# Kernel tuning notes

Hardware: AMD Instinct MI355X
Metric: run time of the kernel (lower is better)

Reference implementation:

```python
import jax, jax.numpy as jnp
import numpy as np

NODE_DIM = 256
HID = 128
EDGE_DIM = 128
NUM_BINS = 22
MAX_LEN = 2056
TOTAL_FEATS = HID * 3 + NUM_BINS * 2 + 2


def get_index_embedding(indices, embed_size, max_len):
    # sinusoidal index embedding as in RiboFlow utils
    K = jnp.arange(embed_size // 2, dtype=jnp.float32)
    ang = indices[..., None].astype(jnp.float32) * jnp.pi / (max_len ** (2.0 * K / embed_size))
    return jnp.concatenate([jnp.sin(ang), jnp.cos(ang)], axis=-1)


def calc_distogram(pos, min_bin, max_bin, num_bins):
    # pos: [B, N, 3] -> one-hot distogram [B, N, N, num_bins]
    d = jnp.linalg.norm(pos[:, :, None, :] - pos[:, None, :, :], axis=-1)[..., None]
    lower = jnp.linspace(min_bin, max_bin, num_bins)
    upper = jnp.concatenate([lower[1:], jnp.array([1e8], dtype=jnp.float32)])
    return ((d > lower) & (d < upper)).astype(jnp.float32)


def cross_concat(f):
    # f: [B, N, D] -> [B, N, N, 2D] via row/col tiling
    B, N, D = f.shape
    return jnp.concatenate([
        jnp.broadcast_to(f[:, :, None, :], (B, N, N, D)),
        jnp.broadcast_to(f[:, None, :, :], (B, N, N, D)),
    ], axis=-1)


def _linear_params(key, fi, fo):
    s = 1.0 / np.sqrt(fi)
    kw, kb = jax.random.split(key)
    W = jax.random.uniform(kw, (fi, fo), jnp.float32, -s, s)
    b = jax.random.uniform(kb, (fo,), jnp.float32, -s, s)
    return W, b


def setup_inputs() -> dict:
    key = jax.random.key(0)
    ks = jax.random.split(key, 12)
    B, N = 1, 512
    inp = {
        'node_features': jax.random.normal(ks[0], (B, N, NODE_DIM), jnp.float32),
        'trans': jax.random.normal(ks[1], (B, N, 3), jnp.float32) * 10.0,
        'sc_trans': jax.random.normal(ks[2], (B, N, 3), jnp.float32) * 10.0,
        'edge_mask': jnp.ones((B, N, N), jnp.float32),
        'flow_mask': (jax.random.uniform(ks[4], (B, N)) > 0.5).astype(jnp.float32),
    }
    inp['W_n2e'], inp['b_n2e'] = _linear_params(ks[5], NODE_DIM, HID)
    inp['W_rp'], inp['b_rp'] = _linear_params(ks[6], HID, HID)
    inp['W1'], inp['b1'] = _linear_params(ks[7], TOTAL_FEATS, EDGE_DIM)
    inp['W2'], inp['b2'] = _linear_params(ks[8], EDGE_DIM, EDGE_DIM)
    inp['W3'], inp['b3'] = _linear_params(ks[9], EDGE_DIM, EDGE_DIM)
    inp['ln_g'] = jnp.ones((EDGE_DIM,), jnp.float32)
    inp['ln_b'] = jnp.zeros((EDGE_DIM,), jnp.float32)
    return inp


def reference(node_features, trans, sc_trans, edge_mask, flow_mask,
              W_n2e, b_n2e, W_rp, b_rp, W1, b1, W2, b2, W3, b3, ln_g, ln_b):
    B, N, _ = node_features.shape
    # node -> edge projection, then cross-concat tiling: [B,N,N,2*HID]
    n2e = node_features @ W_n2e + b_n2e
    pair_node_feats = cross_concat(n2e)
    # relative position sinusoidal embedding + linear: [B,N,N,HID]
    seq = jnp.arange(N, dtype=jnp.float32)
    relpos = jnp.broadcast_to(seq[None, :, None] - seq[None, None, :], (B, N, N))
    relpos_feats = get_index_embedding(relpos, HID, MAX_LEN) @ W_rp + b_rp
    # distograms: [B,N,N,NUM_BINS] each
    dist_feats = calc_distogram(trans, 0.001, 20.0, NUM_BINS)
    sc_feats = calc_distogram(sc_trans, 0.001, 20.0, NUM_BINS)
    # flow mask pair features: [B,N,N,2]
    flow_feat = cross_concat(flow_mask[..., None])
    feats = jnp.concatenate([pair_node_feats, relpos_feats, dist_feats, sc_feats, flow_feat], axis=-1)
    # 3-layer MLP + LayerNorm
    h = jax.nn.relu(feats @ W1 + b1)
    h = jax.nn.relu(h @ W2 + b2)
    h = h @ W3 + b3
    mu = jnp.mean(h, axis=-1, keepdims=True)
    var = jnp.var(h, axis=-1, keepdims=True)
    h = (h - mu) * jax.lax.rsqrt(var + 1e-5) * ln_g + ln_b
    return h * edge_mask[..., None]
```

## Files before the change

kernel.cpp:

```cpp
#include <hip/hip_runtime.h>


using bf16x8 = __attribute__((ext_vector_type(8))) short;
using f32x4  = __attribute__((ext_vector_type(4))) float;

__device__ __forceinline__ unsigned short f2bf(float f) {
    unsigned int u;
    __builtin_memcpy(&u, &f, 4);
    unsigned int r = (u + 0x7fffu + ((u >> 16) & 1u)) >> 16;
    return (unsigned short)r;
}

__device__ __forceinline__ unsigned int cvt_pk_bf16(float lo, float hi) {
    unsigned int r;
    asm("v_cvt_pk_bf16_f32 %0, %1, %2" : "=v"(r) : "v"(lo), "v"(hi));
    return r;
}

__global__ void pre_all(const float* __restrict__ nf,
                        const float* __restrict__ Wn2e,
                        const float* __restrict__ bn2e,
                        const float* __restrict__ W1,
                        const float* __restrict__ b1,
                        const float* __restrict__ flow,
                        const float* __restrict__ Wrp,
                        const float* __restrict__ brp,
                        const float* __restrict__ W2,
                        const float* __restrict__ W3,
                        float* __restrict__ A, float* __restrict__ Bv,
                        float* __restrict__ Rm,
                        short* __restrict__ W2b, short* __restrict__ W3b)
{
    __shared__ float s0[256];
    __shared__ float s1[128];
    const int bid = blockIdx.x;
    const int m = threadIdx.x;

    if (bid < 512) {
        const int i = bid;
        s0[m]       = nf[i * 256 + m];
        s0[m + 128] = nf[i * 256 + 128 + m];
        __syncthreads();
        float c0 = 0.f, c1 = 0.f, c2 = 0.f, c3 = 0.f;
        #pragma unroll 4
        for (int k = 0; k < 256; k += 4) {
            c0 += s0[k + 0] * Wn2e[(k + 0) * 128 + m];
            c1 += s0[k + 1] * Wn2e[(k + 1) * 128 + m];
            c2 += s0[k + 2] * Wn2e[(k + 2) * 128 + m];
            c3 += s0[k + 3] * Wn2e[(k + 3) * 128 + m];
        }
        s1[m] = bn2e[m] + ((c0 + c1) + (c2 + c3));
        __syncthreads();
        const float fl = flow[i];
        float aA0 = b1[m] + fl * W1[428 * 128 + m], aA1 = 0.f;
        float aB0 =         fl * W1[429 * 128 + m], aB1 = 0.f;
        #pragma unroll 4
        for (int k = 0; k < 128; k += 2) {
            aA0 += s1[k]     * W1[(k) * 128 + m];
            aA1 += s1[k + 1] * W1[(k + 1) * 128 + m];
            aB0 += s1[k]     * W1[(128 + k) * 128 + m];
            aB1 += s1[k + 1] * W1[(129 + k) * 128 + m];
        }
        A[i * 128 + m]  = aA0 + aA1;
        Bv[i * 128 + m] = aB0 + aB1;
    } else if (bid < 1535) {
        const int dix = bid - 512;
        const float d = (float)(dix - 511);
        const int K = m & 63;
        const float denom = powf(2056.0f, (float)K * (1.0f / 64.0f));
        const float ang = d * 3.14159265358979323846f / denom;
        s0[m] = (m < 64) ? sinf(ang) : cosf(ang);
        __syncthreads();
        float c0 = 0.f, c1 = 0.f, c2 = 0.f, c3 = 0.f;
        #pragma unroll 4
        for (int k = 0; k < 128; k += 4) {
            c0 += s0[k + 0] * Wrp[(k + 0) * 128 + m];
            c1 += s0[k + 1] * Wrp[(k + 1) * 128 + m];
            c2 += s0[k + 2] * Wrp[(k + 2) * 128 + m];
            c3 += s0[k + 3] * Wrp[(k + 3) * 128 + m];
        }
        s1[m] = brp[m] + ((c0 + c1) + (c2 + c3));
        __syncthreads();
        c0 = 0.f; c1 = 0.f; c2 = 0.f; c3 = 0.f;
        #pragma unroll 4
        for (int k = 0; k < 128; k += 4) {
            c0 += s1[k + 0] * W1[(256 + k) * 128 + m];
            c1 += s1[k + 1] * W1[(257 + k) * 128 + m];
            c2 += s1[k + 2] * W1[(258 + k) * 128 + m];
            c3 += s1[k + 3] * W1[(259 + k) * 128 + m];
        }
        Rm[dix * 128 + m] = (c0 + c1) + (c2 + c3);
    } else {
        const int t = (bid - 1535) * 128 + m;
        for (int h = 0; h < 2; h++) {
            const int idx = t + h * 8192;
            const int k = idx >> 7, n = idx & 127;
            const int dst = ((k >> 3) * 128 + n) * 8 + (k & 7);
            W2b[dst] = (short)f2bf(W2[idx]);
            W3b[dst] = (short)f2bf(W3[idx]);
        }
    }
}

__global__ __launch_bounds__(512, 4) void edge_main(
    const float* __restrict__ trans,
    const float* __restrict__ sctrans,
    const float* __restrict__ emask,
    const float* __restrict__ W1,
    const short* __restrict__ W2b,
    const float* __restrict__ b2,
    const short* __restrict__ W3b,
    const float* __restrict__ b3,
    const float* __restrict__ lng,
    const float* __restrict__ lnb,
    const float* __restrict__ A,
    const float* __restrict__ Bv,
    const float* __restrict__ Rm,
    float* __restrict__ out)
{
    __shared__ __align__(16) short W2L[16384];
    __shared__ __align__(16) short W3L[16384];
    __shared__ __align__(16) float As[128];
    __shared__ int binsD[256];
    __shared__ int binsS[256];

    const int tid = threadIdx.x;
    const int i  = blockIdx.x >> 1;
    const int j0 = (blockIdx.x & 1) << 8;

    for (int r = 0; r < 4; r++) {
        const int off = (r * 512 + tid) * 16;
        __builtin_amdgcn_global_load_lds(
            (const __attribute__((address_space(1))) void*)((const char*)W2b + off),
            (__attribute__((address_space(3))) void*)((char*)W2L + off), 16, 0, 0);
        __builtin_amdgcn_global_load_lds(
            (const __attribute__((address_space(1))) void*)((const char*)W3b + off),
            (__attribute__((address_space(3))) void*)((char*)W3L + off), 16, 0, 0);
    }

    if (tid < 128) As[tid] = A[i * 128 + tid];

    {
        const int p = tid & 255;
        const float* P = (tid < 256) ? trans : sctrans;
        const int j = j0 + p;
        const float dx = __fsub_rn(P[i * 3 + 0], P[j * 3 + 0]);
        const float dy = __fsub_rn(P[i * 3 + 1], P[j * 3 + 1]);
        const float dz = __fsub_rn(P[i * 3 + 2], P[j * 3 + 2]);
        const float d2 = __fadd_rn(__fadd_rn(__fmul_rn(dx, dx), __fmul_rn(dy, dy)),
                                   __fmul_rn(dz, dz));
        const double dd = (double)sqrtf(d2);
        const double step = (20.0 - 0.001) / 21.0;
        int bin = -1;
        for (int b = 0; b < 22; b++) {
            const double lo = (b == 21) ? 20.0 : __dadd_rn(0.001, __dmul_rn((double)b, step));
            const double up = (b == 20) ? 20.0 :
                              ((b == 21) ? 1e8 : __dadd_rn(0.001, __dmul_rn((double)(b + 1), step)));
            if (dd > lo && dd < up) bin = b;
        }
        if (tid < 256) binsD[p] = bin; else binsS[p] = bin;
    }
    __syncthreads();

    const int w = tid >> 6;
    const int l = tid & 63;
    const int q = l >> 4;
    const int ln16 = l & 15;

    const f32x4 vzero = {0.0f, 0.0f, 0.0f, 0.0f};
    const int laA = (((q & 1) * 2) * 16 + ln16) * 4;
    const int laB = laA + 64;
    const bool selHi = (q >> 1) != 0;

    for (int mt = 0; mt < 2; mt++) {
        const int p = 32 * w + mt * 16 + ln16;
        const int j = j0 + p;

        bf16x8 af[4];
        {
            const int didx = i - j + 511;
            const int bD = binsD[p], bS = binsS[p];
            const float sD = bD >= 0 ? 1.0f : 0.0f;
            const float sS = bS >= 0 ? 1.0f : 0.0f;
            const int rD = 384 + (bD >= 0 ? bD : 0);
            const int rS = 406 + (bS >= 0 ? bS : 0);
            const float* __restrict__ BvR = &Bv[j * 128];
            const float* __restrict__ RmR = &Rm[didx * 128];
            const float* __restrict__ WdR = &W1[rD * 128];
            const float* __restrict__ WsR = &W1[rS * 128];
            #pragma unroll
            for (int kb = 0; kb < 4; kb++) {
                const int f0 = kb * 32 + q * 8;
                const f32x4 bv0 = *(const f32x4*)&BvR[f0];
                const f32x4 bv1 = *(const f32x4*)&BvR[f0 + 4];
                const f32x4 r0  = *(const f32x4*)&RmR[f0];
                const f32x4 r1  = *(const f32x4*)&RmR[f0 + 4];
                const f32x4 a0  = *(const f32x4*)&As[f0];
                const f32x4 a1  = *(const f32x4*)&As[f0 + 4];
                const f32x4 w0  = *(const f32x4*)&WdR[f0];
                const f32x4 w1  = *(const f32x4*)&WdR[f0 + 4];
                const f32x4 s0  = *(const f32x4*)&WsR[f0];
                const f32x4 s1  = *(const f32x4*)&WsR[f0 + 4];
                float h[8];
                #pragma unroll
                for (int e = 0; e < 4; e++) {
                    h[e]     = fmaxf(a0[e] + bv0[e] + r0[e] + sD * w0[e] + sS * s0[e], 0.0f);
                    h[e + 4] = fmaxf(a1[e] + bv1[e] + r1[e] + sD * w1[e] + sS * s1[e], 0.0f);
                }
                union { unsigned int u[4]; bf16x8 v; } cv;
                cv.u[0] = cvt_pk_bf16(h[0], h[1]);
                cv.u[1] = cvt_pk_bf16(h[2], h[3]);
                cv.u[2] = cvt_pk_bf16(h[4], h[5]);
                cv.u[3] = cvt_pk_bf16(h[6], h[7]);
                af[kb] = cv.v;
            }
        }

        unsigned int P[8][2];
        #pragma unroll
        for (int nt = 0; nt < 8; nt++) {
            f32x4 acc2 = vzero;
            #pragma unroll
            for (int kb = 0; kb < 4; kb++) {
                const bf16x8 wf = *(const bf16x8*)&W2L[((kb * 4 + q) * 128 + nt * 16 + ln16) * 8];
                acc2 = __builtin_amdgcn_mfma_f32_16x16x32_bf16(wf, af[kb], acc2, 0, 0, 0);
            }
            const f32x4 b2c = *(const f32x4*)&b2[nt * 16 + q * 4];
            P[nt][0] = cvt_pk_bf16(fmaxf(acc2[0] + b2c[0], 0.0f),
                                   fmaxf(acc2[1] + b2c[1], 0.0f));
            P[nt][1] = cvt_pk_bf16(fmaxf(acc2[2] + b2c[2], 0.0f),
                                   fmaxf(acc2[3] + b2c[3], 0.0f));
        }

        f32x4 acc3[8];
        #pragma unroll
        for (int nt = 0; nt < 8; nt++) acc3[nt] = vzero;
        #pragma unroll
        for (int kb = 0; kb < 4; kb++) {
            const int r0a = __builtin_amdgcn_ds_bpermute(laA, (int)P[2 * kb][0]);
            const int r1a = __builtin_amdgcn_ds_bpermute(laA, (int)P[2 * kb][1]);
            const int r2a = __builtin_amdgcn_ds_bpermute(laB, (int)P[2 * kb][0]);
            const int r3a = __builtin_amdgcn_ds_bpermute(laB, (int)P[2 * kb][1]);
            const int r0b = __builtin_amdgcn_ds_bpermute(laA, (int)P[2 * kb + 1][0]);
            const int r1b = __builtin_amdgcn_ds_bpermute(laA, (int)P[2 * kb + 1][1]);
            const int r2b = __builtin_amdgcn_ds_bpermute(laB, (int)P[2 * kb + 1][0]);
            const int r3b = __builtin_amdgcn_ds_bpermute(laB, (int)P[2 * kb + 1][1]);
            union { unsigned int u[4]; bf16x8 v; } bf;
            bf.u[0] = (unsigned int)(selHi ? r0b : r0a);
            bf.u[1] = (unsigned int)(selHi ? r1b : r1a);
            bf.u[2] = (unsigned int)(selHi ? r2b : r2a);
            bf.u[3] = (unsigned int)(selHi ? r3b : r3a);
            #pragma unroll
            for (int nt = 0; nt < 8; nt++) {
                const bf16x8 wf = *(const bf16x8*)&W3L[((kb * 4 + q) * 128 + nt * 16 + ln16) * 8];
                acc3[nt] = __builtin_amdgcn_mfma_f32_16x16x32_bf16(wf, bf.v, acc3[nt], 0, 0, 0);
            }
        }

        float s = 0.0f;
        #pragma unroll
        for (int nt = 0; nt < 8; nt++) {
            const f32x4 b3c = *(const f32x4*)&b3[nt * 16 + q * 4];
            #pragma unroll
            for (int rg = 0; rg < 4; rg++) {
                acc3[nt][rg] += b3c[rg];
                s += acc3[nt][rg];
            }
        }
        s += __shfl_xor(s, 16, 64);
        s += __shfl_xor(s, 32, 64);
        const float mu = s * (1.0f / 128.0f);
        float ss = 0.0f;
        #pragma unroll
        for (int nt = 0; nt < 8; nt++)
            #pragma unroll
            for (int rg = 0; rg < 4; rg++) {
                const float dv = acc3[nt][rg] - mu;
                ss += dv * dv;
            }
        ss += __shfl_xor(ss, 16, 64);
        ss += __shfl_xor(ss, 32, 64);
        const float rstd = rsqrtf(ss * (1.0f / 128.0f) + 1e-5f);
        const float msk = emask[i * 512 + j];
        float* __restrict__ orow = &out[(i * 512 + j) * 128];
        #pragma unroll
        for (int nt = 0; nt < 8; nt++) {
            const f32x4 gc = *(const f32x4*)&lng[nt * 16 + q * 4];
            const f32x4 bc = *(const f32x4*)&lnb[nt * 16 + q * 4];
            f32x4 o;
            #pragma unroll
            for (int rg = 0; rg < 4; rg++)
                o[rg] = ((acc3[nt][rg] - mu) * rstd * gc[rg] + bc[rg]) * msk;
            *(f32x4*)&orow[nt * 16 + q * 4] = o;
        }
    }
}

extern "C" void kernel_launch(void* const* d_in, const int* in_sizes, int n_in,
                              void* d_out, int out_size, void* d_ws, size_t ws_size,
                              hipStream_t stream)
{
    const float* nf    = (const float*)d_in[0];
    const float* trans = (const float*)d_in[1];
    const float* sctr  = (const float*)d_in[2];
    const float* emask = (const float*)d_in[3];
    const float* flow  = (const float*)d_in[4];
    const float* Wn2e  = (const float*)d_in[5];
    const float* bn2e  = (const float*)d_in[6];
    const float* Wrp   = (const float*)d_in[7];
    const float* brp   = (const float*)d_in[8];
    const float* W1    = (const float*)d_in[9];
    const float* b1    = (const float*)d_in[10];
    const float* W2    = (const float*)d_in[11];
    const float* b2    = (const float*)d_in[12];
    const float* W3    = (const float*)d_in[13];
    const float* b3    = (const float*)d_in[14];
    const float* lng   = (const float*)d_in[15];
    const float* lnb   = (const float*)d_in[16];

    float* ws = (float*)d_ws;
    float* A   = ws;
    float* Bv  = ws + 512 * 128;
    float* Rm  = ws + 2 * 512 * 128;
    short* W2b = (short*)(ws + 262016);
    short* W3b = (short*)(ws + 270208);
    float* out = (float*)d_out;

    pre_all<<<1599, 128, 0, stream>>>(nf, Wn2e, bn2e, W1, b1, flow, Wrp, brp,
                                      W2, W3, A, Bv, Rm, W2b, W3b);
    edge_main<<<1024, 512, 0, stream>>>(trans, sctr, emask, W1, W2b, b2, W3b, b3,
                                        lng, lnb, A, Bv, Rm, out);
}
```

Measured before the change: 251.5 us.

## Restructure preprocessing kernel with split-K reduction across 512-thread blocks

Replaces the 1599-block, 128-thread preprocessing kernel with 512 blocks of 512 threads. Each block handles one node row, two relative-position rows and a slice of the W2/W3 bf16 conversion. The matvecs are split four ways over K and reduced through shared memory, which shortens each thread's serial dependent chain. The cost is extra barriers and a reduction step, and the preprocessing kernel is a small part of the total next to edge_main.

```diff
diff --git a/kernel.cpp b/kernel.cpp
--- a/kernel.cpp
+++ b/kernel.cpp
@@ -17,88 +17,113 @@
     return r;
 }
 
-__global__ void pre_all(const float* __restrict__ nf,
-                        const float* __restrict__ Wn2e,
-                        const float* __restrict__ bn2e,
-                        const float* __restrict__ W1,
-                        const float* __restrict__ b1,
-                        const float* __restrict__ flow,
-                        const float* __restrict__ Wrp,
-                        const float* __restrict__ brp,
-                        const float* __restrict__ W2,
-                        const float* __restrict__ W3,
-                        float* __restrict__ A, float* __restrict__ Bv,
-                        float* __restrict__ Rm,
-                        short* __restrict__ W2b, short* __restrict__ W3b)
+__global__ __launch_bounds__(512) void pre_fast(
+    const float* __restrict__ nf,
+    const float* __restrict__ flow,
+    const float* __restrict__ Wn2e,
+    const float* __restrict__ bn2e,
+    const float* __restrict__ Wrp,
+    const float* __restrict__ brp,
+    const float* __restrict__ W1,
+    const float* __restrict__ b1,
+    const float* __restrict__ W2,
+    const float* __restrict__ W3,
+    float* __restrict__ Aw, float* __restrict__ Bv,
+    float* __restrict__ Rm,
+    short* __restrict__ W2b, short* __restrict__ W3b)
 {
-    __shared__ float s0[256];
-    __shared__ float s1[128];
+    __shared__ float nfs[256];
+    __shared__ float n2s[128];
+    __shared__ float red[512];
+    __shared__ float emb[128];
+    __shared__ float rp[128];
+
     const int bid = blockIdx.x;
-    const int m = threadIdx.x;
-
-    if (bid < 512) {
-        const int i = bid;
-        s0[m]       = nf[i * 256 + m];
-        s0[m + 128] = nf[i * 256 + 128 + m];
-        __syncthreads();
-        float c0 = 0.f, c1 = 0.f, c2 = 0.f, c3 = 0.f;
-        #pragma unroll 4
-        for (int k = 0; k < 256; k += 4) {
-            c0 += s0[k + 0] * Wn2e[(k + 0) * 128 + m];
-            c1 += s0[k + 1] * Wn2e[(k + 1) * 128 + m];
-            c2 += s0[k + 2] * Wn2e[(k + 2) * 128 + m];
-            c3 += s0[k + 3] * Wn2e[(k + 3) * 128 + m];
-        }
-        s1[m] = bn2e[m] + ((c0 + c1) + (c2 + c3));
-        __syncthreads();
-        const float fl = flow[i];
-        float aA0 = b1[m] + fl * W1[428 * 128 + m], aA1 = 0.f;
-        float aB0 =         fl * W1[429 * 128 + m], aB1 = 0.f;
-        #pragma unroll 4
-        for (int k = 0; k < 128; k += 2) {
-            aA0 += s1[k]     * W1[(k) * 128 + m];
-            aA1 += s1[k + 1] * W1[(k + 1) * 128 + m];
-            aB0 += s1[k]     * W1[(128 + k) * 128 + m];
-            aB1 += s1[k + 1] * W1[(129 + k) * 128 + m];
-        }
-        A[i * 128 + m]  = aA0 + aA1;
-        Bv[i * 128 + m] = aB0 + aB1;
-    } else if (bid < 1535) {
-        const int dix = bid - 512;
+    const int tid = threadIdx.x;
+    const int i = bid;
+    const int m = tid & 127, ks = tid >> 7;
+
+    if (tid < 64) {
+        const int idx = bid * 64 + tid;
+        const int v   = idx & 16383;
+        const int k   = v >> 7, n = v & 127;
+        const int dst = ((k >> 3) * 128 + n) * 8 + (k & 7);
+        if (idx < 16384) W2b[dst] = (short)f2bf(W2[v]);
+        else             W3b[dst] = (short)f2bf(W3[v]);
+    }
+
+    if (tid < 256) nfs[tid] = nf[i * 256 + tid];
+    __syncthreads();
+    {
+        float p0 = 0.f, p1 = 0.f;
+        #pragma unroll 8
+        for (int k = ks * 64; k < ks * 64 + 64; k += 2) {
+            p0 += nfs[k]     * Wn2e[k * 128 + m];
+            p1 += nfs[k + 1] * Wn2e[(k + 1) * 128 + m];
+        }
+        red[tid] = p0 + p1;
+    }
+    __syncthreads();
+    if (tid < 128)
+        n2s[tid] = bn2e[tid] +
+                   ((red[tid] + red[tid + 128]) + (red[tid + 256] + red[tid + 384]));
+    __syncthreads();
+
+    {
+        float pa = 0.f, pb = 0.f;
+        #pragma unroll 8
+        for (int k = ks * 32; k < ks * 32 + 32; k++) {
+            const float s = n2s[k];
+            pa += s * W1[k * 128 + m];
+            pb += s * W1[(128 + k) * 128 + m];
+        }
+        red[tid] = pa;
+        __syncthreads();
+        float pA = 0.f;
+        if (tid < 128)
+            pA = (red[tid] + red[tid + 128]) + (red[tid + 256] + red[tid + 384]);
+        __syncthreads();
+        red[tid] = pb;
+        __syncthreads();
+        if (tid < 128) {
+            const float fl = flow[i];
+            Aw[i * 128 + tid] = pA + b1[tid] + fl * W1[428 * 128 + tid];
+            Bv[i * 128 + tid] =
+                (red[tid] + red[tid + 128]) + (red[tid + 256] + red[tid + 384]) +
+                fl * W1[429 * 128 + tid];
+        }
+    }
+    __syncthreads();
+
+    for (int rr = 0; rr < 2; rr++) {
+        const int dix = bid * 2 + rr;
+        if (dix > 1022) break;
         const float d = (float)(dix - 511);
-        const int K = m & 63;
-        const float denom = powf(2056.0f, (float)K * (1.0f / 64.0f));
-        const float ang = d * 3.14159265358979323846f / denom;
-        s0[m] = (m < 64) ? sinf(ang) : cosf(ang);
-        __syncthreads();
-        float c0 = 0.f, c1 = 0.f, c2 = 0.f, c3 = 0.f;
-        #pragma unroll 4
-        for (int k = 0; k < 128; k += 4) {
-            c0 += s0[k + 0] * Wrp[(k + 0) * 128 + m];
-            c1 += s0[k + 1] * Wrp[(k + 1) * 128 + m];
-            c2 += s0[k + 2] * Wrp[(k + 2) * 128 + m];
-            c3 += s0[k + 3] * Wrp[(k + 3) * 128 + m];
-        }
-        s1[m] = brp[m] + ((c0 + c1) + (c2 + c3));
-        __syncthreads();
-        c0 = 0.f; c1 = 0.f; c2 = 0.f; c3 = 0.f;
-        #pragma unroll 4
-        for (int k = 0; k < 128; k += 4) {
-            c0 += s1[k + 0] * W1[(256 + k) * 128 + m];
-            c1 += s1[k + 1] * W1[(257 + k) * 128 + m];
-            c2 += s1[k + 2] * W1[(258 + k) * 128 + m];
-            c3 += s1[k + 3] * W1[(259 + k) * 128 + m];
-        }
-        Rm[dix * 128 + m] = (c0 + c1) + (c2 + c3);
-    } else {
-        const int t = (bid - 1535) * 128 + m;
-        for (int h = 0; h < 2; h++) {
-            const int idx = t + h * 8192;
-            const int k = idx >> 7, n = idx & 127;
-            const int dst = ((k >> 3) * 128 + n) * 8 + (k & 7);
-            W2b[dst] = (short)f2bf(W2[idx]);
-            W3b[dst] = (short)f2bf(W3[idx]);
-        }
+        if (tid < 128) {
+            const int K = tid & 63;
+            const float denom = powf(2056.0f, (float)K * (1.0f / 64.0f));
+            const float ang = d * 3.14159265358979323846f / denom;
+            emb[tid] = (tid < 64) ? sinf(ang) : cosf(ang);
+        }
+        __syncthreads();
+        float p = 0.f;
+        #pragma unroll 8
+        for (int k = ks * 32; k < ks * 32 + 32; k++) p += emb[k] * Wrp[k * 128 + m];
+        red[tid] = p;
+        __syncthreads();
+        if (tid < 128)
+            rp[tid] = brp[tid] +
+                      ((red[tid] + red[tid + 128]) + (red[tid + 256] + red[tid + 384]));
+        __syncthreads();
+        p = 0.f;
+        #pragma unroll 8
+        for (int k = ks * 32; k < ks * 32 + 32; k++) p += rp[k] * W1[(256 + k) * 128 + m];
+        red[tid] = p;
+        __syncthreads();
+        if (tid < 128)
+            Rm[dix * 128 + tid] =
+                (red[tid] + red[tid + 128]) + (red[tid + 256] + red[tid + 384]);
+        __syncthreads();
     }
 }
 
@@ -319,15 +344,15 @@
     const float* lnb   = (const float*)d_in[16];
 
     float* ws = (float*)d_ws;
-    float* A   = ws;
-    float* Bv  = ws + 512 * 128;
-    float* Rm  = ws + 2 * 512 * 128;
+    float* Aw  = ws;
+    float* Bv  = ws + 65536;
+    float* Rm  = ws + 131072;
     short* W2b = (short*)(ws + 262016);
     short* W3b = (short*)(ws + 270208);
     float* out = (float*)d_out;
 
-    pre_all<<<1599, 128, 0, stream>>>(nf, Wn2e, bn2e, W1, b1, flow, Wrp, brp,
-                                      W2, W3, A, Bv, Rm, W2b, W3b);
+    pre_fast<<<512, 512, 0, stream>>>(nf, flow, Wn2e, bn2e, Wrp, brp, W1, b1,
+                                      W2, W3, Aw, Bv, Rm, W2b, W3b);
     edge_main<<<1024, 512, 0, stream>>>(trans, sctr, emask, W1, W2b, b2, W3b, b3,
-                                        lng, lnb, A, Bv, Rm, out);
-}
+                                        lng, lnb, Aw, Bv, Rm, out);
+}
```

Measured after the change: 249.9 us. About the same (-0.6%).
